# Kernel optimization log

Hardware: AMD Instinct MI355X
Metric: run time of the kernel (lower is better)

## Reference

```python
import jax, jax.numpy as jnp
import numpy as np

BN_EPS = 1e-5
LRELU_SLOPE = 0.01  # torch nn.LeakyReLU default


def setup_inputs() -> dict:
    key = jax.random.key(0)
    k1, k2 = jax.random.split(key)
    B, N, Cin, Cout = 8, 4096, 64, 128
    x = jax.random.normal(k1, (B, N, Cin), dtype=jnp.float32)
    W = jax.random.normal(k2, (Cout, Cin), dtype=jnp.float32) * (1.0 / np.sqrt(Cin))
    gamma = jnp.ones((Cout,), dtype=jnp.float32)
    beta = jnp.zeros((Cout,), dtype=jnp.float32)
    return {"x": x, "W": W, "gamma": gamma, "beta": beta, "k": 8}


def _knn_gather_max(x, k):
    # x: [B, N, C]. Negative squared euclidean distance (larger = closer).
    xx = jnp.sum(x * x, axis=-1)                       # [B, N]
    inner = jnp.einsum('bnc,bmc->bnm', x, x)           # [B, N, N]
    neg_dist = 2.0 * inner - xx[:, :, None] - xx[:, None, :]
    idx = jax.lax.top_k(neg_dist, k)[1]                # [B, N, k] int32
    # gather neighbor features: neigh[b,n,j,c] = x[b, idx[b,n,j], c]
    neigh = jax.vmap(lambda xb, ib: xb[ib])(x, idx)    # [B, N, k, C]
    return jnp.max(neigh, axis=2)                      # [B, N, C]


def reference(x, W, gamma, beta, k):
    feat = _knn_gather_max(x, k)                       # [B, N, Cin]
    y = jnp.einsum('bnc,oc->bno', feat, W)             # 1x1 Conv1d, no bias -> [B, N, Cout]
    # BatchNorm1d in training mode: stats over batch and spatial (N) dims
    mean = jnp.mean(y, axis=(0, 1))
    var = jnp.var(y, axis=(0, 1))
    y = (y - mean) * jax.lax.rsqrt(var + BN_EPS) * gamma + beta
    return jnp.where(y >= 0, y, LRELU_SLOPE * y)       # LeakyReLU
```

## Files before the change

kernel.cpp:

```cpp
#include <hip/hip_runtime.h>
#include <hip/hip_bf16.h>

#define NPTS 4096
#define CIN 64
#define COUT 128
#define BATCH 8
#define KNN 8
#define NCH 12
#define NCT 24
#define TOTROWS (BATCH * NPTS)

using short8 = __attribute__((ext_vector_type(8))) short;
using f32x4  = __attribute__((ext_vector_type(4))) float;

__device__ __forceinline__ unsigned short f2bf_rne(float f) {
    unsigned int u = __float_as_uint(f);
    unsigned int r = (u + 0x7fffu + ((u >> 16) & 1u)) >> 16;
    return (unsigned short)r;
}

__device__ __forceinline__ unsigned int umed3(unsigned int a, unsigned int b, unsigned int c) {
    unsigned int d;
    asm("v_med3_u32 %0, %1, %2, %3" : "=v"(d) : "v"(a), "v"(b), "v"(c));
    return d;
}

__global__ __launch_bounds__(256) void prep_kernel(const float* __restrict__ x,
                                                   unsigned short* __restrict__ xpack,
                                                   float* __restrict__ xxn,
                                                   double* __restrict__ xxd) {
    int i   = blockIdx.x * 256 + threadIdx.x;
    int row = i >> 3, g = i & 7;
    const float* src = x + (size_t)row * CIN + g * 8;
    float4 v0 = *(const float4*)src;
    float4 v1 = *(const float4*)(src + 4);
    float f[8] = {v0.x, v0.y, v0.z, v0.w, v1.x, v1.y, v1.z, v1.w};

    unsigned int h[8];
    double s = 0.0;
    #pragma unroll
    for (int j = 0; j < 8; ++j) {
        h[j] = (unsigned int)f2bf_rne(f[j]);
        s += (double)f[j] * (double)f[j];
    }
    uint4 hi;
    hi.x = h[0] | (h[1] << 16); hi.y = h[2] | (h[3] << 16);
    hi.z = h[4] | (h[5] << 16); hi.w = h[6] | (h[7] << 16);
    *(uint4*)&xpack[(size_t)row * 64 + g * 8] = hi;

    s += __shfl_xor(s, 1);
    s += __shfl_xor(s, 2);
    s += __shfl_xor(s, 4);
    if (g == 0) { xxn[row] = 1000.f - (float)s; xxd[row] = s; }
}

__global__ __launch_bounds__(256, 4) void knn_cand_kernel(const unsigned short* __restrict__ xpack,
                                                          const float* __restrict__ xxn,
                                                          int* __restrict__ cand) {
    __shared__ __align__(16) unsigned int mK[8192];
    __shared__ float xxs[256];
    unsigned short* BUF0 = (unsigned short*)mK;
    unsigned short* BUF1 = BUF0 + 8192;

    const int tid  = threadIdx.x;
    const int n0   = blockIdx.x * 64;
    const int half = blockIdx.y;
    const int b    = blockIdx.z;
    const int wave = tid >> 6;
    const int lane = tid & 63;
    const int lrow = lane & 15;
    const int quad = lane >> 4;
    const int colbase = half << 11;

    const unsigned short* xp = xpack + ((size_t)b << 12) * 64;
    const float* xnn = xxn + (b << 12);

    const int arow = n0 + wave * 16 + lrow;
    short8 ah0 = *(const short8*)&xp[arow * 64 + quad * 8];
    short8 ah1 = *(const short8*)&xp[arow * 64 + 32 + quad * 8];

    unsigned int keys[4][8];
    #pragma unroll
    for (int r = 0; r < 4; ++r)
        #pragma unroll
        for (int j = 0; j < 8; ++j) keys[r][j] = 0u;

    uint4 pr[4]; float pxv;
    int swi[4];
    #pragma unroll
    for (int k = 0; k < 4; ++k) {
        int G = k * 256 + tid, row = G >> 3, h = G & 7;
        swi[k] = row * 64 + ((h ^ (row & 7)) << 3);
    }

    {
        const size_t base0 = (size_t)colbase * 64;
        #pragma unroll
        for (int k = 0; k < 4; ++k) {
            int G = k * 256 + tid;
            pr[k] = *(const uint4*)&xp[base0 + G * 8];
        }
        pxv = (tid < 128) ? xnn[colbase + tid] : 0.f;
        #pragma unroll
        for (int k = 0; k < 4; ++k)
            *(uint4*)&BUF0[swi[k]] = pr[k];
        if (tid < 128) xxs[tid] = pxv;
    }
    __syncthreads();

    for (int ot = 0; ot < 16; ++ot) {
        unsigned short* cur = (ot & 1) ? BUF1 : BUF0;
        unsigned short* nxt = (ot & 1) ? BUF0 : BUF1;
        const float*    xs  = xxs + (ot & 1) * 128;

        if (ot < 15) {
            const size_t base = (size_t)(colbase + (ot + 1) * 128) * 64;
            #pragma unroll
            for (int k = 0; k < 4; ++k) {
                int G = k * 256 + tid;
                pr[k] = *(const uint4*)&xp[base + G * 8];
            }
            if (tid < 128) pxv = xnn[colbase + (ot + 1) * 128 + tid];
        }

        #pragma unroll 4
        for (int p2 = 0; p2 < 8; ++p2) {
            const int row0 = p2 * 16 + lrow;
            const int s    = lrow & 7;
            short8 bh0 = *(const short8*)&cur[row0 * 64 + ((quad ^ s) << 3)];
            short8 bh1 = *(const short8*)&cur[row0 * 64 + (((4 + quad) ^ s) << 3)];
            const float xm = xs[row0];
            f32x4 acc = {0.f, 0.f, 0.f, 0.f};
            acc = __builtin_amdgcn_mfma_f32_16x16x32_bf16(ah0, bh0, acc, 0, 0, 0);
            acc = __builtin_amdgcn_mfma_f32_16x16x32_bf16(ah1, bh1, acc, 0, 0, 0);
            const unsigned int pp = (unsigned int)(ot * 8 + p2);
            #pragma unroll
            for (int r = 0; r < 4; ++r) {
                float v = fmaf(acc[r], 2.f, xm);
                unsigned int t = (__float_as_uint(v) & 0xFFFFFF80u) | pp;
                #pragma unroll
                for (int j = 7; j >= 1; --j)
                    keys[r][j] = umed3(keys[r][j - 1], keys[r][j], t);
                keys[r][0] = keys[r][0] > t ? keys[r][0] : t;
            }
        }

        if (ot < 15) {
            #pragma unroll
            for (int k = 0; k < 4; ++k)
                *(uint4*)&nxt[swi[k]] = pr[k];
            if (tid < 128) xxs[(1 - (ot & 1)) * 128 + tid] = pxv;
        }
        __syncthreads();
    }

    const int mrow = wave * 16 + quad * 4;
    #pragma unroll
    for (int r = 0; r < 4; ++r) {
        uint4 k0 = make_uint4(keys[r][0], keys[r][1], keys[r][2], keys[r][3]);
        uint4 k1 = make_uint4(keys[r][4], keys[r][5], keys[r][6], keys[r][7]);
        *(uint4*)&mK[(mrow + r) * 128 + lrow * 8]     = k0;
        *(uint4*)&mK[(mrow + r) * 128 + lrow * 8 + 4] = k1;
    }
    __syncthreads();

    if (tid < 64) {
        unsigned int bk[NCH]; int bc[NCH];
        #pragma unroll
        for (int j = 0; j < NCH; ++j) { bk[j] = 0u; bc[j] = 0; }
        const unsigned int* rowK = mK + tid * 128;
        for (int c = 0; c < 128; ++c) {
            int pos = (tid + c) & 127;
            unsigned int k = rowK[pos];
            if (k > bk[NCH - 1]) {
                int lr = pos >> 3;
                int p  = (int)(k & 0x7Fu);
                int col = (half << 11) + (p << 4) + lr;
                bk[NCH - 1] = k; bc[NCH - 1] = col;
                #pragma unroll
                for (int j = NCH - 1; j > 0; --j) {
                    if (bk[j] > bk[j - 1]) {
                        unsigned int tk = bk[j]; bk[j] = bk[j - 1]; bk[j - 1] = tk;
                        int tc = bc[j]; bc[j] = bc[j - 1]; bc[j - 1] = tc;
                    }
                }
            }
        }
        int* co = cand + ((size_t)((b << 12) + n0 + tid)) * NCT + half * NCH;
        #pragma unroll
        for (int j = 0; j < NCH; ++j) co[j] = bc[j];
    }
}

__global__ __launch_bounds__(256) void rerank_kernel(const float* __restrict__ x,
                                                     const double* __restrict__ xxd,
                                                     const int* __restrict__ cand,
                                                     float* __restrict__ feat) {
    __shared__ double sc[4][NCT];
    __shared__ int    si[4][NCT];
    __shared__ int    sel[4][KNN];
    const int tid = threadIdx.x, wave = tid >> 6, lane = tid & 63;
    const size_t row = (size_t)blockIdx.x * 4 + wave;
    const int b = (int)(row >> 12);
    const float* xb = x + (((size_t)b) << 12) * CIN;
    const float* xn = x + row * CIN;

    const int cidx = lane & 31, part = lane >> 5;
    if (cidx < NCT) {
        int m = cand[row * NCT + cidx];
        const float* xm = xb + (size_t)m * CIN;
        const float* xa = xn + part * 32;
        const float* xv = xm + part * 32;
        double a0 = 0.0, a1 = 0.0, a2 = 0.0, a3 = 0.0;
        #pragma unroll
        for (int c4 = 0; c4 < 8; c4 += 4) {
            float4 p0 = *(const float4*)&xa[(c4 + 0) * 4];
            float4 q0 = *(const float4*)&xv[(c4 + 0) * 4];
            float4 p1 = *(const float4*)&xa[(c4 + 1) * 4];
            float4 q1 = *(const float4*)&xv[(c4 + 1) * 4];
            float4 p2 = *(const float4*)&xa[(c4 + 2) * 4];
            float4 q2 = *(const float4*)&xv[(c4 + 2) * 4];
            float4 p3 = *(const float4*)&xa[(c4 + 3) * 4];
            float4 q3 = *(const float4*)&xv[(c4 + 3) * 4];
            a0 = fma((double)p0.x, (double)q0.x, a0); a0 = fma((double)p0.y, (double)q0.y, a0);
            a0 = fma((double)p0.z, (double)q0.z, a0); a0 = fma((double)p0.w, (double)q0.w, a0);
            a1 = fma((double)p1.x, (double)q1.x, a1); a1 = fma((double)p1.y, (double)q1.y, a1);
            a1 = fma((double)p1.z, (double)q1.z, a1); a1 = fma((double)p1.w, (double)q1.w, a1);
            a2 = fma((double)p2.x, (double)q2.x, a2); a2 = fma((double)p2.y, (double)q2.y, a2);
            a2 = fma((double)p2.z, (double)q2.z, a2); a2 = fma((double)p2.w, (double)q2.w, a2);
            a3 = fma((double)p3.x, (double)q3.x, a3); a3 = fma((double)p3.y, (double)q3.y, a3);
            a3 = fma((double)p3.z, (double)q3.z, a3); a3 = fma((double)p3.w, (double)q3.w, a3);
        }
        double d = (a0 + a1) + (a2 + a3);
        d += __shfl_xor(d, 32);
        if (part == 0) {
            sc[wave][cidx] = 2.0 * d - xxd[(((size_t)b) << 12) + m];
            si[wave][cidx] = m;
        }
    }
    __syncthreads();

    if (lane < NCT) {
        double myv = sc[wave][lane];
        int    mym = si[wave][lane];
        int rank = 0;
        #pragma unroll
        for (int c = 0; c < NCT; ++c) {
            double v = sc[wave][c];
            int    m = si[wave][c];
            rank += (v > myv || (v == myv && m < mym)) ? 1 : 0;
        }
        if (rank < KNN) sel[wave][rank] = mym;
    }
    __syncthreads();

    float mx = -3.0e38f;
    #pragma unroll
    for (int j = 0; j < KNN; ++j)
        mx = fmaxf(mx, xb[(size_t)sel[wave][j] * CIN + lane]);
    feat[row * CIN + lane] = mx;
}

__global__ __launch_bounds__(256) void conv_stats_kernel(const float* __restrict__ feat,
                                                         const float* __restrict__ W,
                                                         float* __restrict__ y,
                                                         float* __restrict__ st) {
    __shared__ float Wt[64 * 128];
    __shared__ float Fs[64 * 64];
    __shared__ float bs[128], bs2[128];
    const int tid = threadIdx.x;
    const int n0  = blockIdx.x * 64;

    for (int i = tid; i < 8192; i += 256) {
        int o = i >> 6, c = i & 63;
        Wt[c * 128 + o] = W[i];
    }
    for (int i = tid; i < 1024; i += 256)
        ((float4*)Fs)[i] = ((const float4*)(feat + (size_t)n0 * CIN))[i];
    if (tid < 128) { bs[tid] = 0.f; bs2[tid] = 0.f; }
    __syncthreads();

    const int og = tid & 31, rg = tid >> 5;
    float ts[4] = {0.f, 0.f, 0.f, 0.f}, ts2[4] = {0.f, 0.f, 0.f, 0.f};
    #pragma unroll
    for (int p = 0; p < 4; ++p) {
        const int r0 = p * 16 + rg * 2;
        float acc0[4] = {0.f, 0.f, 0.f, 0.f}, acc1[4] = {0.f, 0.f, 0.f, 0.f};
        for (int c = 0; c < 64; ++c) {
            float f0 = Fs[r0 * 64 + c], f1 = Fs[(r0 + 1) * 64 + c];
            #pragma unroll
            for (int j = 0; j < 4; ++j) {
                float w = Wt[c * 128 + og + 32 * j];
                acc0[j] += f0 * w; acc1[j] += f1 * w;
            }
        }
        #pragma unroll
        for (int j = 0; j < 4; ++j) {
            const int ch = og + 32 * j;
            y[(size_t)(n0 + r0)     * COUT + ch] = acc0[j];
            y[(size_t)(n0 + r0 + 1) * COUT + ch] = acc1[j];
            ts[j]  += acc0[j] + acc1[j];
            ts2[j] += acc0[j] * acc0[j] + acc1[j] * acc1[j];
        }
    }
    #pragma unroll
    for (int j = 0; j < 4; ++j) {
        atomicAdd(&bs [og + 32 * j], ts[j]);
        atomicAdd(&bs2[og + 32 * j], ts2[j]);
    }
    __syncthreads();
    if (tid < 128) {
        atomicAdd(&st[tid],       bs[tid]);
        atomicAdd(&st[128 + tid], bs2[tid]);
    }
}

__global__ __launch_bounds__(256) void norm_out_kernel(const float* __restrict__ y,
                                                       const float* __restrict__ st,
                                                       const float* __restrict__ gamma,
                                                       const float* __restrict__ beta,
                                                       float* __restrict__ out) {
    size_t i = ((size_t)blockIdx.x * 256 + threadIdx.x) * 4;
    int c0 = (int)(i & 127);
    float4 v = *(const float4*)&y[i];
    float o[4];
    const float inv = 1.0f / (float)TOTROWS;
    #pragma unroll
    for (int j = 0; j < 4; ++j) {
        int c = c0 + j;
        float m  = st[c] * inv;
        float vr = st[128 + c] * inv - m * m;
        float sc = rsqrtf(vr + 1e-5f) * gamma[c];
        float t  = (((const float*)&v)[j] - m) * sc + beta[c];
        o[j] = (t >= 0.f) ? t : 0.01f * t;
    }
    *(float4*)&out[i] = make_float4(o[0], o[1], o[2], o[3]);
}

extern "C" void kernel_launch(void* const* d_in, const int* in_sizes, int n_in,
                              void* d_out, int out_size, void* d_ws, size_t ws_size,
                              hipStream_t stream) {
    (void)in_sizes; (void)n_in; (void)out_size; (void)ws_size;
    const float* x     = (const float*)d_in[0];
    const float* W     = (const float*)d_in[1];
    const float* gamma = (const float*)d_in[2];
    const float* beta  = (const float*)d_in[3];
    float* out = (float*)d_out;

    char*   ws    = (char*)d_ws;
    float*  xxn   = (float*)ws;
    double* xxd   = (double*)(ws + 131072);
    int*    cand  = (int*)(ws + 131072 + 262144);
    float*  feat  = (float*)(ws + 131072 + 262144 + 4194304);
    unsigned short* xpack = (unsigned short*)(ws + 131072 + 262144 + 4194304 + 8388608);
    float*  y     = (float*)xpack;
    float*  st    = (float*)(ws + 131072 + 262144 + 4194304 + 8388608 + 16777216);

    hipMemsetAsync(st, 0, 256 * sizeof(float), stream);
    prep_kernel      <<<TOTROWS * 8 / 256, 256, 0, stream>>>(x, xpack, xxn, xxd);
    knn_cand_kernel  <<<dim3(NPTS / 64, 2, BATCH), 256, 0, stream>>>(xpack, xxn, cand);
    rerank_kernel    <<<TOTROWS / 4, 256, 0, stream>>>(x, xxd, cand, feat);
    conv_stats_kernel<<<TOTROWS / 64, 256, 0, stream>>>(feat, W, y, st);
    norm_out_kernel  <<<(TOTROWS * COUT) / (256 * 4), 256, 0, stream>>>(y, st, gamma, beta, out);
}
```

Baseline: 295.8 us.

## Split KNN candidate column tiles across two wave groups per block

The KNN candidate kernel now runs 512 threads per block: the original four row-waves are duplicated into two column-slice groups, each handling alternating 16-column subtiles of every 128-column tile. Each group keeps its own per-lane top-8 keys, and the two groups' key sets are merged in two sequential passes through shared memory by the first 64 threads. This doubles the waves available to hide MFMA and med3 latency and halves the serial insertion work per wave. The cost is an extra merge pass and two extra barriers, and occupancy depends on whether 8 waves per SIMD fit the register budget.

```diff
diff --git a/kernel.cpp b/kernel.cpp
--- a/kernel.cpp
+++ b/kernel.cpp
@@ -54,7 +54,7 @@
     if (g == 0) { xxn[row] = 1000.f - (float)s; xxd[row] = s; }
 }
 
-__global__ __launch_bounds__(256, 4) void knn_cand_kernel(const unsigned short* __restrict__ xpack,
+__global__ __launch_bounds__(512, 8) void knn_cand_kernel(const unsigned short* __restrict__ xpack,
                                                           const float* __restrict__ xxn,
                                                           int* __restrict__ cand) {
     __shared__ __align__(16) unsigned int mK[8192];
@@ -70,12 +70,14 @@
     const int lane = tid & 63;
     const int lrow = lane & 15;
     const int quad = lane >> 4;
+    const int rg   = wave & 3;
+    const int cs   = wave >> 2;
     const int colbase = half << 11;
 
     const unsigned short* xp = xpack + ((size_t)b << 12) * 64;
     const float* xnn = xxn + (b << 12);
 
-    const int arow = n0 + wave * 16 + lrow;
+    const int arow = n0 + rg * 16 + lrow;
     short8 ah0 = *(const short8*)&xp[arow * 64 + quad * 8];
     short8 ah1 = *(const short8*)&xp[arow * 64 + 32 + quad * 8];
 
@@ -85,24 +87,24 @@
         #pragma unroll
         for (int j = 0; j < 8; ++j) keys[r][j] = 0u;
 
-    uint4 pr[4]; float pxv;
-    int swi[4];
-    #pragma unroll
-    for (int k = 0; k < 4; ++k) {
-        int G = k * 256 + tid, row = G >> 3, h = G & 7;
+    uint4 pr[2]; float pxv;
+    int swi[2];
+    #pragma unroll
+    for (int k = 0; k < 2; ++k) {
+        int G = k * 512 + tid, row = G >> 3, h = G & 7;
         swi[k] = row * 64 + ((h ^ (row & 7)) << 3);
     }
 
     {
         const size_t base0 = (size_t)colbase * 64;
         #pragma unroll
-        for (int k = 0; k < 4; ++k) {
-            int G = k * 256 + tid;
+        for (int k = 0; k < 2; ++k) {
+            int G = k * 512 + tid;
             pr[k] = *(const uint4*)&xp[base0 + G * 8];
         }
         pxv = (tid < 128) ? xnn[colbase + tid] : 0.f;
         #pragma unroll
-        for (int k = 0; k < 4; ++k)
+        for (int k = 0; k < 2; ++k)
             *(uint4*)&BUF0[swi[k]] = pr[k];
         if (tid < 128) xxs[tid] = pxv;
     }
@@ -116,15 +118,16 @@
         if (ot < 15) {
             const size_t base = (size_t)(colbase + (ot + 1) * 128) * 64;
             #pragma unroll
-            for (int k = 0; k < 4; ++k) {
-                int G = k * 256 + tid;
+            for (int k = 0; k < 2; ++k) {
+                int G = k * 512 + tid;
                 pr[k] = *(const uint4*)&xp[base + G * 8];
             }
             if (tid < 128) pxv = xnn[colbase + (ot + 1) * 128 + tid];
         }
 
-        #pragma unroll 4
-        for (int p2 = 0; p2 < 8; ++p2) {
+        #pragma unroll
+        for (int i = 0; i < 4; ++i) {
+            const int p2   = 2 * i + cs;
             const int row0 = p2 * 16 + lrow;
             const int s    = lrow & 7;
             short8 bh0 = *(const short8*)&cur[row0 * 64 + ((quad ^ s) << 3)];
@@ -147,27 +150,31 @@
 
         if (ot < 15) {
             #pragma unroll
-            for (int k = 0; k < 4; ++k)
+            for (int k = 0; k < 2; ++k)
                 *(uint4*)&nxt[swi[k]] = pr[k];
             if (tid < 128) xxs[(1 - (ot & 1)) * 128 + tid] = pxv;
         }
         __syncthreads();
     }
 
-    const int mrow = wave * 16 + quad * 4;
-    #pragma unroll
-    for (int r = 0; r < 4; ++r) {
-        uint4 k0 = make_uint4(keys[r][0], keys[r][1], keys[r][2], keys[r][3]);
-        uint4 k1 = make_uint4(keys[r][4], keys[r][5], keys[r][6], keys[r][7]);
-        *(uint4*)&mK[(mrow + r) * 128 + lrow * 8]     = k0;
-        *(uint4*)&mK[(mrow + r) * 128 + lrow * 8 + 4] = k1;
-    }
-    __syncthreads();
+    const int mrow = rg * 16 + quad * 4;
+
+    if (cs == 0) {
+        #pragma unroll
+        for (int r = 0; r < 4; ++r) {
+            uint4 k0 = make_uint4(keys[r][0], keys[r][1], keys[r][2], keys[r][3]);
+            uint4 k1 = make_uint4(keys[r][4], keys[r][5], keys[r][6], keys[r][7]);
+            *(uint4*)&mK[(mrow + r) * 128 + lrow * 8]     = k0;
+            *(uint4*)&mK[(mrow + r) * 128 + lrow * 8 + 4] = k1;
+        }
+    }
+    __syncthreads();
+
+    unsigned int bk[NCH]; int bc[NCH];
+    #pragma unroll
+    for (int j = 0; j < NCH; ++j) { bk[j] = 0u; bc[j] = 0; }
 
     if (tid < 64) {
-        unsigned int bk[NCH]; int bc[NCH];
-        #pragma unroll
-        for (int j = 0; j < NCH; ++j) { bk[j] = 0u; bc[j] = 0; }
         const unsigned int* rowK = mK + tid * 128;
         for (int c = 0; c < 128; ++c) {
             int pos = (tid + c) & 127;
@@ -186,6 +193,39 @@
                 }
             }
         }
+    }
+    __syncthreads();
+
+    if (cs == 1) {
+        #pragma unroll
+        for (int r = 0; r < 4; ++r) {
+            uint4 k0 = make_uint4(keys[r][0], keys[r][1], keys[r][2], keys[r][3]);
+            uint4 k1 = make_uint4(keys[r][4], keys[r][5], keys[r][6], keys[r][7]);
+            *(uint4*)&mK[(mrow + r) * 128 + lrow * 8]     = k0;
+            *(uint4*)&mK[(mrow + r) * 128 + lrow * 8 + 4] = k1;
+        }
+    }
+    __syncthreads();
+
+    if (tid < 64) {
+        const unsigned int* rowK = mK + tid * 128;
+        for (int c = 0; c < 128; ++c) {
+            int pos = (tid + c) & 127;
+            unsigned int k = rowK[pos];
+            if (k > bk[NCH - 1]) {
+                int lr = pos >> 3;
+                int p  = (int)(k & 0x7Fu);
+                int col = (half << 11) + (p << 4) + lr;
+                bk[NCH - 1] = k; bc[NCH - 1] = col;
+                #pragma unroll
+                for (int j = NCH - 1; j > 0; --j) {
+                    if (bk[j] > bk[j - 1]) {
+                        unsigned int tk = bk[j]; bk[j] = bk[j - 1]; bk[j - 1] = tk;
+                        int tc = bc[j]; bc[j] = bc[j - 1]; bc[j - 1] = tc;
+                    }
+                }
+            }
+        }
         int* co = cand + ((size_t)((b << 12) + n0 + tid)) * NCT + half * NCH;
         #pragma unroll
         for (int j = 0; j < NCH; ++j) co[j] = bc[j];
@@ -358,7 +398,7 @@
 
     hipMemsetAsync(st, 0, 256 * sizeof(float), stream);
     prep_kernel      <<<TOTROWS * 8 / 256, 256, 0, stream>>>(x, xpack, xxn, xxd);
-    knn_cand_kernel  <<<dim3(NPTS / 64, 2, BATCH), 256, 0, stream>>>(xpack, xxn, cand);
+    knn_cand_kernel  <<<dim3(NPTS / 64, 2, BATCH), 512, 0, stream>>>(xpack, xxn, cand);
     rerank_kernel    <<<TOTROWS / 4, 256, 0, stream>>>(x, xxd, cand, feat);
     conv_stats_kernel<<<TOTROWS / 64, 256, 0, stream>>>(feat, W, y, st);
     norm_out_kernel  <<<(TOTROWS * COUT) / (256 * 4), 256, 0, stream>>>(y, st, gamma, beta, out);
```

After: 410.0 us. +38.6%, slower.
